# Kernel tuning notes

Measured on AMD Instinct MI355X. Metric: run time of the kernel, lower is better.

The kernel has to match this reference:

```python
import jax, jax.numpy as jnp
import numpy as np


def setup_inputs() -> dict:
    key = jax.random.key(0)
    k1, k2 = jax.random.split(key)
    B, Lq, Ls, D = 16, 2048, 2048, 512
    query = jax.random.normal(k1, (B, Lq, D), dtype=jnp.float32)
    support = jax.random.normal(k2, (B, Ls, D), dtype=jnp.float32)
    return {"query": query, "support": support}


def reference(query, support):
    # attn: [B, Lq, Ls] = softmax(query @ support^T, axis=-1)
    logits = jnp.einsum("bqd,bsd->bqs", query, support)
    attn = jax.nn.softmax(logits, axis=-1)
    # attended support: [B, Lq, D]
    attended = jnp.einsum("bqs,bsd->bqd", attn, support)
    # score: [B, Lq] = sum over D of query * attended
    score = jnp.sum(query * attended, axis=-1)
    return score
```

## Files before the change

kernel.cpp:

```cpp
#include <hip/hip_runtime.h>
#include <hip/hip_bf16.h>

#define B_  16
#define LQ  2048
#define LS  2048
#define DD  512
#define BQ  256
#define BS  256
#define BK  64
#define NSB (LS / BS)
#define NKC (DD / BK)
#define NSPLIT 2

typedef short bf16x8 __attribute__((ext_vector_type(8)));
typedef float f32x4  __attribute__((ext_vector_type(4)));

__device__ __forceinline__ void load_lds16(const void* g, void* l) {
  __builtin_amdgcn_global_load_lds((const __attribute__((address_space(1))) void*)g,
                                   (__attribute__((address_space(3))) void*)l,
                                   16, 0, 0);
}

__device__ __forceinline__ unsigned short f2bf(float f) {
  union { float f; unsigned int u; } v; v.f = f;
  unsigned int r = v.u + 0x7fffu + ((v.u >> 16) & 1u);
  return (unsigned short)(r >> 16);
}

__global__ __launch_bounds__(256) void cvt_kernel(const float* __restrict__ Q,
                                                  const float* __restrict__ S,
                                                  unsigned short* __restrict__ Qw,
                                                  unsigned short* __restrict__ Sw,
                                                  int nblk) {
  int blk = blockIdx.x;
  const float* src; unsigned short* dst;
  if (blk < nblk) { src = Q; dst = Qw; } else { src = S; dst = Sw; blk -= nblk; }
  int i = blk * 256 + threadIdx.x;
  float4 f = ((const float4*)src)[i];
  ushort4 u;
  u.x = f2bf(f.x); u.y = f2bf(f.y); u.z = f2bf(f.z); u.w = f2bf(f.w);
  ((ushort4*)dst)[i] = u;
}

__global__ __launch_bounds__(1024, 4) void attn_kernel(const unsigned short* __restrict__ Qw,
                                                       const unsigned short* __restrict__ Sw,
                                                       float* __restrict__ pm,
                                                       float* __restrict__ pse,
                                                       float* __restrict__ psel) {
  __shared__ __align__(16) unsigned short sQ[2][BQ * BK];
  __shared__ __align__(16) unsigned short sS[2][BS * BK];

  const int id   = blockIdx.x;
  const int qb   = id >> 5;
  const int bs   = id & 31;
  const int b    = bs >> 1;
  const int spl  = bs & 1;
  const int tid  = threadIdx.x;
  const int w    = tid >> 6;
  const int lane = tid & 63;
  const int h    = w & 3;
  const int g    = w >> 2;
  const int col  = lane & 15;
  const int quad = lane >> 4;
  const int c7   = col & 7;

  const int q0 = qb * BQ;
  const unsigned short* Qb = Qw + (size_t)b * LQ * DD;
  const unsigned short* Sb = Sw + (size_t)b * LS * DD;

  float mst[4] = { -INFINITY, -INFINITY, -INFINITY, -INFINITY };
  float se[4]  = { 0.f, 0.f, 0.f, 0.f };
  float sel[4] = { 0.f, 0.f, 0.f, 0.f };

  f32x4 acc[4][4];

  const int rr = lane >> 3;
  const int cc = ((lane & 7) ^ rr) * 8;

  const int sbp = NSB / NSPLIT;
  const int sbs = spl * sbp;
  const int T   = sbp * NKC;

  auto issue = [&](int t, int buf) {
    const int kb = (t & 7) * BK + cc;
    if (w < 8) {
      const int r0 = w * 32;
#pragma unroll
      for (int i = 0; i < 4; ++i)
        load_lds16(Qb + (size_t)(q0 + r0 + i * 8 + rr) * DD + kb, &sQ[buf][(r0 + i * 8) * BK]);
    } else {
      const int s0 = (sbs + (t >> 3)) * BS + (w - 8) * 32;
      const int l0 = (w - 8) * 32;
#pragma unroll
      for (int i = 0; i < 4; ++i)
        load_lds16(Sb + (size_t)(s0 + i * 8 + rr) * DD + kb, &sS[buf][(l0 + i * 8) * BK]);
    }
  };

  issue(0, 0);

  for (int t = 0; t < T; ++t) {
    const int buf = t & 1;
    __syncthreads();
    if (t + 1 < T) issue(t + 1, buf ^ 1);

    if ((t & 7) == 0) {
#pragma unroll
      for (int st = 0; st < 4; ++st)
#pragma unroll
        for (int qt = 0; qt < 4; ++qt)
          acc[st][qt] = (f32x4){0.f, 0.f, 0.f, 0.f};
    }

#pragma unroll
    for (int kk = 0; kk < 2; ++kk) {
      const int koff = ((kk * 4 + quad) ^ c7) * 8;
      bf16x8 aq[4], asv[4];
#pragma unroll
      for (int qt = 0; qt < 4; ++qt)
        aq[qt] = *(const bf16x8*)&sQ[buf][(g * 64 + qt * 16 + col) * BK + koff];
#pragma unroll
      for (int st = 0; st < 4; ++st)
        asv[st] = *(const bf16x8*)&sS[buf][(h * 64 + st * 16 + col) * BK + koff];
#pragma unroll
      for (int st = 0; st < 4; ++st)
#pragma unroll
        for (int qt = 0; qt < 4; ++qt)
          acc[st][qt] = __builtin_amdgcn_mfma_f32_16x16x32_bf16(asv[st], aq[qt], acc[st][qt], 0, 0, 0);
    }

    if ((t & 7) == 7) {
#pragma unroll
      for (int qt = 0; qt < 4; ++qt) {
        float lmax = mst[qt];
#pragma unroll
        for (int st = 0; st < 4; ++st)
#pragma unroll
          for (int r = 0; r < 4; ++r)
            lmax = fmaxf(lmax, acc[st][qt][r]);
        lmax = fmaxf(lmax, __shfl_xor(lmax, 16, 64));
        lmax = fmaxf(lmax, __shfl_xor(lmax, 32, 64));
        float alpha = __expf(mst[qt] - lmax);
        float pe = 0.f, pel = 0.f;
#pragma unroll
        for (int st = 0; st < 4; ++st)
#pragma unroll
          for (int r = 0; r < 4; ++r) {
            float l = acc[st][qt][r];
            float e = __expf(l - lmax);
            pe += e;
            pel = fmaf(e, l, pel);
          }
        pe  += __shfl_xor(pe, 16, 64);  pe  += __shfl_xor(pe, 32, 64);
        pel += __shfl_xor(pel, 16, 64); pel += __shfl_xor(pel, 32, 64);
        se[qt]  = fmaf(se[qt],  alpha, pe);
        sel[qt] = fmaf(sel[qt], alpha, pel);
        mst[qt] = lmax;
      }
    }
  }

  __syncthreads();
  float* red = (float*)&sQ[0][0];
  if (quad == 0) {
#pragma unroll
    for (int qt = 0; qt < 4; ++qt) {
      int idx = ((g * 4 + h) * 4 + qt) * 16 + col;
      red[idx]        = mst[qt];
      red[1024 + idx] = se[qt];
      red[2048 + idx] = sel[qt];
    }
  }
  __syncthreads();
  if (h == 0 && quad == 0) {
#pragma unroll
    for (int qt = 0; qt < 4; ++qt) {
      float M = -INFINITY;
#pragma unroll
      for (int hh = 0; hh < 4; ++hh)
        M = fmaxf(M, red[((g * 4 + hh) * 4 + qt) * 16 + col]);
      float SE = 0.f, SEL = 0.f;
#pragma unroll
      for (int hh = 0; hh < 4; ++hh) {
        int idx = ((g * 4 + hh) * 4 + qt) * 16 + col;
        float a = __expf(red[idx] - M);
        SE  = fmaf(red[1024 + idx], a, SE);
        SEL = fmaf(red[2048 + idx], a, SEL);
      }
      size_t qi = (size_t)b * LQ + q0 + g * 64 + qt * 16 + col;
      pm[qi * NSPLIT + spl]   = M;
      pse[qi * NSPLIT + spl]  = SE;
      psel[qi * NSPLIT + spl] = SEL;
    }
  }
}

__global__ __launch_bounds__(256) void combine_kernel(const float* __restrict__ pm,
                                                      const float* __restrict__ pse,
                                                      const float* __restrict__ psel,
                                                      float* __restrict__ out) {
  int i = blockIdx.x * blockDim.x + threadIdx.x;
  if (i >= B_ * LQ) return;
  float M = -INFINITY;
#pragma unroll
  for (int s = 0; s < NSPLIT; ++s) M = fmaxf(M, pm[i * NSPLIT + s]);
  float SE = 0.f, SEL = 0.f;
#pragma unroll
  for (int s = 0; s < NSPLIT; ++s) {
    float a = __expf(pm[i * NSPLIT + s] - M);
    SE  = fmaf(pse[i * NSPLIT + s],  a, SE);
    SEL = fmaf(psel[i * NSPLIT + s], a, SEL);
  }
  out[i] = SEL / SE;
}

__global__ __launch_bounds__(256) void fallback_kernel(const float* __restrict__ Q,
                                                       const float* __restrict__ S,
                                                       float* __restrict__ out) {
  __shared__ float qv[DD];
  __shared__ float red[256];
  const int b = blockIdx.y, qi = blockIdx.x, tid = threadIdx.x;
  const float* qrow = Q + ((size_t)b * LQ + qi) * DD;
  for (int d = tid; d < DD; d += 256) qv[d] = qrow[d];
  __syncthreads();
  const float* Sb = S + (size_t)b * LS * DD;
  float m = -INFINITY, se = 0.f, sel = 0.f;
  for (int s = tid; s < LS; s += 256) {
    const float* srow = Sb + (size_t)s * DD;
    float dot = 0.f;
    for (int d = 0; d < DD; ++d) dot = fmaf(qv[d], srow[d], dot);
    float mn = fmaxf(m, dot);
    float a = __expf(m - mn);
    float e = __expf(dot - mn);
    se  = se * a + e;
    sel = sel * a + e * dot;
    m = mn;
  }
  red[tid] = m; __syncthreads();
  for (int o = 128; o > 0; o >>= 1) { if (tid < o) red[tid] = fmaxf(red[tid], red[tid + o]); __syncthreads(); }
  float M = red[0]; __syncthreads();
  float a = __expf(m - M); se *= a; sel *= a;
  red[tid] = se; __syncthreads();
  for (int o = 128; o > 0; o >>= 1) { if (tid < o) red[tid] += red[tid + o]; __syncthreads(); }
  float SE = red[0]; __syncthreads();
  red[tid] = sel; __syncthreads();
  for (int o = 128; o > 0; o >>= 1) { if (tid < o) red[tid] += red[tid + o]; __syncthreads(); }
  float SEL = red[0];
  if (tid == 0) out[(size_t)b * LQ + qi] = SEL / SE;
}

extern "C" void kernel_launch(void* const* d_in, const int* in_sizes, int n_in,
                              void* d_out, int out_size, void* d_ws, size_t ws_size,
                              hipStream_t stream) {
  const float* Q = (const float*)d_in[0];
  const float* S = (const float*)d_in[1];
  float* out = (float*)d_out;
  const size_t nelem = (size_t)B_ * LQ * DD;
  const size_t part_elems = (size_t)B_ * LQ * NSPLIT;
  const size_t need = 2 * nelem * sizeof(unsigned short)
                    + 3 * part_elems * sizeof(float);

  if (ws_size >= need) {
    unsigned short* Qw = (unsigned short*)d_ws;
    unsigned short* Sw = Qw + nelem;
    float* pm   = (float*)(Sw + nelem);
    float* pse  = pm + part_elems;
    float* psel = pse + part_elems;
    int nblk = (int)(nelem / 4 / 256);
    cvt_kernel<<<2 * nblk, 256, 0, stream>>>(Q, S, Qw, Sw, nblk);
    attn_kernel<<<(LQ / BQ) * B_ * NSPLIT, 1024, 0, stream>>>(Qw, Sw, pm, pse, psel);
    combine_kernel<<<(B_ * LQ + 255) / 256, 256, 0, stream>>>(pm, pse, psel, out);
  } else {
    fallback_kernel<<<dim3(LQ, B_), 256, 0, stream>>>(Q, S, out);
  }
}
```

Baseline: 238.0 us.

## Deepen attention load pipeline to four LDS stages with manual waitcnt barriers

Halves the K-chunk to 32 and replaces the double-buffered LDS scheme with a four-buffer ring. Loads are issued three stages ahead, and each step synchronises with an explicit s_waitcnt vmcnt plus s_barrier instead of __syncthreads, so global-to-LDS latency is better hidden behind MFMA work. The load mapping and XOR swizzle are reworked so each wave issues one 16-byte load per operand per stage. The conversion kernel now also handles 8 elements per thread with 16-byte stores. The cost is twice as many barriers per tile and some redundant clamped loads past the final stage.

```diff
diff --git a/kernel.cpp b/kernel.cpp
--- a/kernel.cpp
+++ b/kernel.cpp
@@ -7,13 +7,15 @@
 #define DD  512
 #define BQ  256
 #define BS  256
-#define BK  64
+#define BK  32
 #define NSB (LS / BS)
 #define NKC (DD / BK)
 #define NSPLIT 2
+#define T_STAGES ((NSB / NSPLIT) * NKC)
 
 typedef short bf16x8 __attribute__((ext_vector_type(8)));
 typedef float f32x4  __attribute__((ext_vector_type(4)));
+typedef unsigned short u16x8 __attribute__((ext_vector_type(8)));
 
 __device__ __forceinline__ void load_lds16(const void* g, void* l) {
   __builtin_amdgcn_global_load_lds((const __attribute__((address_space(1))) void*)g,
@@ -36,10 +38,12 @@
   const float* src; unsigned short* dst;
   if (blk < nblk) { src = Q; dst = Qw; } else { src = S; dst = Sw; blk -= nblk; }
   int i = blk * 256 + threadIdx.x;
-  float4 f = ((const float4*)src)[i];
-  ushort4 u;
-  u.x = f2bf(f.x); u.y = f2bf(f.y); u.z = f2bf(f.z); u.w = f2bf(f.w);
-  ((ushort4*)dst)[i] = u;
+  float4 f0 = ((const float4*)src)[i * 2];
+  float4 f1 = ((const float4*)src)[i * 2 + 1];
+  u16x8 u;
+  u[0] = f2bf(f0.x); u[1] = f2bf(f0.y); u[2] = f2bf(f0.z); u[3] = f2bf(f0.w);
+  u[4] = f2bf(f1.x); u[5] = f2bf(f1.y); u[6] = f2bf(f1.z); u[7] = f2bf(f1.w);
+  ((u16x8*)dst)[i] = u;
 }
 
 __global__ __launch_bounds__(1024, 4) void attn_kernel(const unsigned short* __restrict__ Qw,
@@ -47,14 +51,16 @@
                                                        float* __restrict__ pm,
                                                        float* __restrict__ pse,
                                                        float* __restrict__ psel) {
-  __shared__ __align__(16) unsigned short sQ[2][BQ * BK];
-  __shared__ __align__(16) unsigned short sS[2][BS * BK];
+  __shared__ __align__(16) unsigned short sQ0[BQ * BK], sS0[BS * BK];
+  __shared__ __align__(16) unsigned short sQ1[BQ * BK], sS1[BS * BK];
+  __shared__ __align__(16) unsigned short sQ2[BQ * BK], sS2[BS * BK];
+  __shared__ __align__(16) unsigned short sQ3[BQ * BK], sS3[BS * BK];
 
   const int id   = blockIdx.x;
   const int qb   = id >> 5;
-  const int bs   = id & 31;
-  const int b    = bs >> 1;
-  const int spl  = bs & 1;
+  const int bsx  = id & 31;
+  const int b    = bsx >> 1;
+  const int spl  = bsx & 1;
   const int tid  = threadIdx.x;
   const int w    = tid >> 6;
   const int lane = tid & 63;
@@ -62,7 +68,6 @@
   const int g    = w >> 2;
   const int col  = lane & 15;
   const int quad = lane >> 4;
-  const int c7   = col & 7;
 
   const int q0 = qb * BQ;
   const unsigned short* Qb = Qw + (size_t)b * LQ * DD;
@@ -71,97 +76,101 @@
   float mst[4] = { -INFINITY, -INFINITY, -INFINITY, -INFINITY };
   float se[4]  = { 0.f, 0.f, 0.f, 0.f };
   float sel[4] = { 0.f, 0.f, 0.f, 0.f };
-
   f32x4 acc[4][4];
 
-  const int rr = lane >> 3;
-  const int cc = ((lane & 7) ^ rr) * 8;
-
-  const int sbp = NSB / NSPLIT;
-  const int sbs = spl * sbp;
-  const int T   = sbp * NKC;
-
-  auto issue = [&](int t, int buf) {
-    const int kb = (t & 7) * BK + cc;
-    if (w < 8) {
-      const int r0 = w * 32;
-#pragma unroll
-      for (int i = 0; i < 4; ++i)
-        load_lds16(Qb + (size_t)(q0 + r0 + i * 8 + rr) * DD + kb, &sQ[buf][(r0 + i * 8) * BK]);
-    } else {
-      const int s0 = (sbs + (t >> 3)) * BS + (w - 8) * 32;
-      const int l0 = (w - 8) * 32;
-#pragma unroll
-      for (int i = 0; i < 4; ++i)
-        load_lds16(Sb + (size_t)(s0 + i * 8 + rr) * DD + kb, &sS[buf][(l0 + i * 8) * BK]);
+  const int qrow   = 16 * w + (lane >> 2);
+  const int cchunk = (lane & 3) ^ ((lane >> 2) & 3) ^ ((lane >> 4) & 3);
+  const int ldsoff = w * 512;
+
+  const int sbs = spl * (NSB / NSPLIT);
+
+  auto issue = [&](int t, unsigned short* bq, unsigned short* bss) {
+    const int ts = t < T_STAGES ? t : T_STAGES - 1;
+    const int kb = (ts & 15) * BK + cchunk * 8;
+    const int s0 = (sbs + (ts >> 4)) * BS;
+    load_lds16(Qb + (size_t)(q0 + qrow) * DD + kb, bq + ldsoff);
+    load_lds16(Sb + (size_t)(s0 + qrow) * DD + kb, bss + ldsoff);
+  };
+
+  const int pos = (quad ^ (col & 3) ^ ((col >> 2) & 3)) * 8;
+
+  auto compute = [&](const unsigned short* bq, const unsigned short* bss) {
+    bf16x8 aq[4], asv[4];
+#pragma unroll
+    for (int qt = 0; qt < 4; ++qt)
+      aq[qt] = *(const bf16x8*)&bq[(g * 64 + qt * 16 + col) * BK + pos];
+#pragma unroll
+    for (int st = 0; st < 4; ++st)
+      asv[st] = *(const bf16x8*)&bss[(h * 64 + st * 16 + col) * BK + pos];
+#pragma unroll
+    for (int st = 0; st < 4; ++st)
+#pragma unroll
+      for (int qt = 0; qt < 4; ++qt)
+        acc[st][qt] = __builtin_amdgcn_mfma_f32_16x16x32_bf16(asv[st], aq[qt], acc[st][qt], 0, 0, 0);
+  };
+
+  auto initacc = [&]() {
+#pragma unroll
+    for (int st = 0; st < 4; ++st)
+#pragma unroll
+      for (int qt = 0; qt < 4; ++qt)
+        acc[st][qt] = (f32x4){0.f, 0.f, 0.f, 0.f};
+  };
+
+  auto epilogue = [&]() {
+#pragma unroll
+    for (int qt = 0; qt < 4; ++qt) {
+      float lmax = mst[qt];
+#pragma unroll
+      for (int st = 0; st < 4; ++st)
+#pragma unroll
+        for (int r = 0; r < 4; ++r)
+          lmax = fmaxf(lmax, acc[st][qt][r]);
+      lmax = fmaxf(lmax, __shfl_xor(lmax, 16, 64));
+      lmax = fmaxf(lmax, __shfl_xor(lmax, 32, 64));
+      float alpha = __expf(mst[qt] - lmax);
+      float pe = 0.f, pel = 0.f;
+#pragma unroll
+      for (int st = 0; st < 4; ++st)
+#pragma unroll
+        for (int r = 0; r < 4; ++r) {
+          float l = acc[st][qt][r];
+          float e = __expf(l - lmax);
+          pe += e;
+          pel = fmaf(e, l, pel);
+        }
+      pe  += __shfl_xor(pe, 16, 64);  pe  += __shfl_xor(pe, 32, 64);
+      pel += __shfl_xor(pel, 16, 64); pel += __shfl_xor(pel, 32, 64);
+      se[qt]  = fmaf(se[qt],  alpha, pe);
+      sel[qt] = fmaf(sel[qt], alpha, pel);
+      mst[qt] = lmax;
     }
   };
 
-  issue(0, 0);
-
-  for (int t = 0; t < T; ++t) {
-    const int buf = t & 1;
-    __syncthreads();
-    if (t + 1 < T) issue(t + 1, buf ^ 1);
-
-    if ((t & 7) == 0) {
-#pragma unroll
-      for (int st = 0; st < 4; ++st)
-#pragma unroll
-        for (int qt = 0; qt < 4; ++qt)
-          acc[st][qt] = (f32x4){0.f, 0.f, 0.f, 0.f};
-    }
-
-#pragma unroll
-    for (int kk = 0; kk < 2; ++kk) {
-      const int koff = ((kk * 4 + quad) ^ c7) * 8;
-      bf16x8 aq[4], asv[4];
-#pragma unroll
-      for (int qt = 0; qt < 4; ++qt)
-        aq[qt] = *(const bf16x8*)&sQ[buf][(g * 64 + qt * 16 + col) * BK + koff];
-#pragma unroll
-      for (int st = 0; st < 4; ++st)
-        asv[st] = *(const bf16x8*)&sS[buf][(h * 64 + st * 16 + col) * BK + koff];
-#pragma unroll
-      for (int st = 0; st < 4; ++st)
-#pragma unroll
-        for (int qt = 0; qt < 4; ++qt)
-          acc[st][qt] = __builtin_amdgcn_mfma_f32_16x16x32_bf16(asv[st], aq[qt], acc[st][qt], 0, 0, 0);
-    }
-
-    if ((t & 7) == 7) {
-#pragma unroll
-      for (int qt = 0; qt < 4; ++qt) {
-        float lmax = mst[qt];
-#pragma unroll
-        for (int st = 0; st < 4; ++st)
-#pragma unroll
-          for (int r = 0; r < 4; ++r)
-            lmax = fmaxf(lmax, acc[st][qt][r]);
-        lmax = fmaxf(lmax, __shfl_xor(lmax, 16, 64));
-        lmax = fmaxf(lmax, __shfl_xor(lmax, 32, 64));
-        float alpha = __expf(mst[qt] - lmax);
-        float pe = 0.f, pel = 0.f;
-#pragma unroll
-        for (int st = 0; st < 4; ++st)
-#pragma unroll
-          for (int r = 0; r < 4; ++r) {
-            float l = acc[st][qt][r];
-            float e = __expf(l - lmax);
-            pe += e;
-            pel = fmaf(e, l, pel);
-          }
-        pe  += __shfl_xor(pe, 16, 64);  pe  += __shfl_xor(pe, 32, 64);
-        pel += __shfl_xor(pel, 16, 64); pel += __shfl_xor(pel, 32, 64);
-        se[qt]  = fmaf(se[qt],  alpha, pe);
-        sel[qt] = fmaf(sel[qt], alpha, pel);
-        mst[qt] = lmax;
-      }
-    }
-  }
+#define STEP(t, RQ, RS, WQ, WS)                                   \
+  do {                                                            \
+    asm volatile("s_waitcnt vmcnt(4)" ::: "memory");              \
+    asm volatile("s_barrier" ::: "memory");                       \
+    issue((t) + 3, WQ, WS);                                       \
+    if (((t) & 15) == 0) initacc();                               \
+    compute(RQ, RS);                                              \
+    if (((t) & 15) == 15) epilogue();                             \
+  } while (0)
+
+  issue(0, sQ0, sS0);
+  issue(1, sQ1, sS1);
+  issue(2, sQ2, sS2);
+
+  for (int tt = 0; tt < T_STAGES; tt += 4) {
+    STEP(tt + 0, sQ0, sS0, sQ3, sS3);
+    STEP(tt + 1, sQ1, sS1, sQ0, sS0);
+    STEP(tt + 2, sQ2, sS2, sQ1, sS1);
+    STEP(tt + 3, sQ3, sS3, sQ2, sS2);
+  }
+#undef STEP
 
   __syncthreads();
-  float* red = (float*)&sQ[0][0];
+  float* red = (float*)&sQ0[0];
   if (quad == 0) {
 #pragma unroll
     for (int qt = 0; qt < 4; ++qt) {
@@ -266,7 +275,7 @@
     float* pm   = (float*)(Sw + nelem);
     float* pse  = pm + part_elems;
     float* psel = pse + part_elems;
-    int nblk = (int)(nelem / 4 / 256);
+    int nblk = (int)(nelem / 8 / 256);
     cvt_kernel<<<2 * nblk, 256, 0, stream>>>(Q, S, Qw, Sw, nblk);
     attn_kernel<<<(LQ / BQ) * B_ * NSPLIT, 1024, 0, stream>>>(Qw, Sw, pm, pse, psel);
     combine_kernel<<<(B_ * LQ + 255) / 256, 256, 0, stream>>>(pm, pse, psel, out);
```

After: 232.6 us. -2.3%, faster.
